# Optimization experiments

Measured on AMD Instinct MI355X. Metric: run time of the kernel, lower is better.

## Reference

```python
import jax, jax.numpy as jnp
import numpy as np

LAMBDA_D = 250.0
POS_MARGIN = 1.0
NEG_MARGIN = 0.2
BLOCK = 8          # block_size in the original
DIST_THRESH = 7.5  # correspondence threshold in pixels
EPS = 1e-12        # F.normalize eps


def _l2_normalize(x, axis):
    # matches torch.nn.functional.normalize: x / max(||x||_2, eps)
    n = jnp.linalg.norm(x, axis=axis, keepdims=True)
    return x / jnp.maximum(n, EPS)


def setup_inputs() -> dict:
    key = jax.random.key(0)
    k1, k2, k3 = jax.random.split(key, 3)
    b, d, hc, wc = 2, 256, 60, 80  # 480x640 image, block 8
    desc = jax.random.normal(k1, (b, d, hc, wc), dtype=jnp.float32)
    wrap_desc = jax.random.normal(k2, (b, d, hc, wc), dtype=jnp.float32)
    # realistic near-identity homographies (random H would warp everything off-image)
    H = jnp.eye(3, dtype=jnp.float32)[None] + 0.02 * jax.random.normal(k3, (b, 3, 3), dtype=jnp.float32)
    return {"desc": desc, "wrap_desc": wrap_desc, "H": H}


def reference(desc, wrap_desc, H):
    b, d, hc, wc = desc.shape
    n = hc * wc

    # cell-center coordinates in (row, col) order, shape (hc, wc, 2)
    coords = jnp.stack(
        jnp.meshgrid(jnp.arange(hc), jnp.arange(wc), indexing="ij"), axis=-1
    ).astype(jnp.float32) * BLOCK + BLOCK // 2

    # homogeneous (x, y, 1) points, shape (n, 3)
    xy1 = jnp.concatenate(
        [coords[..., 1:2], coords[..., 0:1], jnp.ones((hc, wc, 1), jnp.float32)],
        axis=-1,
    ).reshape(n, 3)

    # warp by homography: (b, n, 3)
    w = jnp.einsum("bij,nj->bni", H, xy1)
    wxy = w[..., :2] / w[..., 2:3]                       # (b, n, 2) in (x, y)
    warp = jnp.stack([wxy[..., 1], wxy[..., 0]], axis=-1).reshape(b, hc, wc, 2)  # (row, col)

    # distance between warped query centers and all cell centers: (b, hc, wc, hc, wc)
    dist = jnp.linalg.norm(coords[None, None, None] - warp[:, :, :, None, None, :], axis=-1)
    S = (dist <= DIST_THRESH).astype(desc.dtype)

    # unit-normalized descriptors, channel-last
    dn = _l2_normalize(jnp.transpose(desc, (0, 2, 3, 1)), axis=-1)       # (b, hc, wc, d)
    wn = _l2_normalize(jnp.transpose(wrap_desc, (0, 2, 3, 1)), axis=-1)  # (b, hc, wc, d)

    # full correlation volume via batched GEMM (same math as broadcast-sum)
    dot = jax.nn.relu(jnp.einsum("bijd,bkld->bijkl", dn, wn))           # (b,hc,wc,hc,wc)

    # normalize over warped-cell axis (k, l), then over query-cell axis (i, j)
    dot = _l2_normalize(dot.reshape(b, hc, wc, n), axis=3).reshape(b, hc, wc, hc, wc)
    dot = _l2_normalize(dot.reshape(b, n, hc, wc), axis=1).reshape(b, hc, wc, hc, wc)

    loss = LAMBDA_D * S * jax.nn.relu(POS_MARGIN - dot) + (1.0 - S) * jax.nn.relu(dot - NEG_MARGIN)
    # sum over (i,j,k,l) per image / n^2, then sum over batch == total sum / n^2
    return jnp.sum(loss) / float(n * n)
```

## Files before the change

kernel.cpp:

```cpp
#include <hip/hip_runtime.h>

#define HC 60
#define WCC 80
#define NCELL 4800
#define NP 4864
#define NB 38
#define DCH 256
#define BATCH 2
#define QT 64

typedef _Float16 half8 __attribute__((ext_vector_type(8)));
typedef float f32x4 __attribute__((ext_vector_type(4)));

__device__ __forceinline__ void gload_lds16(const void* gp, void* lp) {
  __builtin_amdgcn_global_load_lds(
      (const __attribute__((address_space(1))) void*)gp,
      (__attribute__((address_space(3))) void*)lp, 16, 0, 0);
}

__global__ __launch_bounds__(256) void warp_kernel(const float* __restrict__ H,
                                                   float* __restrict__ wout) {
  int idx = blockIdx.x * 256 + threadIdx.x;
  if (idx >= BATCH * NP) return;
  int b = idx / NP;
  int q = idx - b * NP;
  float wr = 1e9f, wc = 1e9f;
  if (q < NCELL) {
    int i = q / WCC;
    int j = q - i * WCC;
    float x = (float)(j * 8 + 4);
    float y = (float)(i * 8 + 4);
    const float* h = H + b * 9;
    float w0 = h[0] * x + h[1] * y + h[2];
    float w1 = h[3] * x + h[4] * y + h[5];
    float w2 = h[6] * x + h[7] * y + h[8];
    wr = w1 / w2;
    wc = w0 / w2;
  }
  wout[2 * idx]     = wr;
  wout[2 * idx + 1] = wc;
}

__global__ __launch_bounds__(256) void normalize_kernel(
    const float* __restrict__ desc, const float* __restrict__ wdesc,
    _Float16* __restrict__ dnp, _Float16* __restrict__ wnp) {
  __shared__ _Float16 vt[DCH][QT + 2];
  __shared__ float pss[4][QT];
  __shared__ float invq[QT];
  const int q0 = blockIdx.x * QT;
  const int which = blockIdx.y;
  const int b = blockIdx.z;
  const float* in = which ? wdesc : desc;
  _Float16* out = which ? wnp : dnp;
  const int tx = threadIdx.x & 63;
  const int ty = threadIdx.x >> 6;
  const int q = q0 + tx;
  float ss = 0.f;
  for (int cc = 0; cc < DCH / 4; ++cc) {
    const int c = cc * 4 + ty;
    float v = (q < NCELL) ? in[((size_t)b * DCH + c) * NCELL + q] : 0.f;
    vt[c][tx] = (_Float16)v;
    ss += v * v;
  }
  pss[ty][tx] = ss;
  __syncthreads();
  if (ty == 0) {
    float tot = pss[0][tx] + pss[1][tx] + pss[2][tx] + pss[3][tx];
    invq[tx] = 1.f / fmaxf(sqrtf(tot), 1e-12f);
  }
  __syncthreads();
  for (int it = 0; it < QT; ++it) {
    out[((size_t)b * NP + q0 + it) * DCH + threadIdx.x] =
        (_Float16)((float)vt[threadIdx.x][it] * invq[it]);
  }
}

template <int MODE>
__global__ __launch_bounds__(256) void gemm_kernel(
    const _Float16* __restrict__ A, const _Float16* __restrict__ Bm,
    const float* __restrict__ invr, const float* __restrict__ colscale,
    const float* __restrict__ warp, float* __restrict__ sqacc,
    float* __restrict__ lossp) {
  __shared__ _Float16 As[128][64];
  __shared__ _Float16 Bs[128][64];
  const int tid = threadIdx.x;
  const int wave = tid >> 6;
  const int lane = tid & 63;
  const int batch = blockIdx.z;
  const int row0 = blockIdx.y * 128;
  const int col0 = blockIdx.x * 128;
  const _Float16* Ab = A + ((size_t)batch * NP + row0) * DCH;
  const _Float16* Bb = Bm + ((size_t)batch * NP + col0) * DCH;

  const int wq_r = wave >> 1;
  const int wq_c = wave & 1;
  const int g = lane >> 4;
  const int cL = lane & 15;

  f32x4 acc[4][4] = {};

  const int srow = lane >> 3;
  const int scol = lane & 7;
  const int sc_swz = (scol ^ srow) * 8;

  for (int ks = 0; ks < 4; ++ks) {
#pragma unroll
    for (int c = 0; c < 4; ++c) {
      const int chunk = wave * 4 + c;
      const int r = chunk * 8 + srow;
      gload_lds16(Ab + (size_t)r * DCH + ks * 64 + sc_swz,
                  (char*)(&As[0][0]) + chunk * 1024);
      gload_lds16(Bb + (size_t)r * DCH + ks * 64 + sc_swz,
                  (char*)(&Bs[0][0]) + chunk * 1024);
    }
    __syncthreads();
#pragma unroll
    for (int kk = 0; kk < 2; ++kk) {
      half8 af[4], bf[4];
#pragma unroll
      for (int m = 0; m < 4; ++m) {
        const int row = wq_r * 64 + m * 16 + cL;
        const int c16 = (kk * 4 + g) ^ (row & 7);
        af[m] = *reinterpret_cast<const half8*>(
            (const char*)(&As[0][0]) + row * 128 + c16 * 16);
      }
#pragma unroll
      for (int n = 0; n < 4; ++n) {
        const int row = wq_c * 64 + n * 16 + cL;
        const int c16 = (kk * 4 + g) ^ (row & 7);
        bf[n] = *reinterpret_cast<const half8*>(
            (const char*)(&Bs[0][0]) + row * 128 + c16 * 16);
      }
#pragma unroll
      for (int m = 0; m < 4; ++m)
#pragma unroll
        for (int n = 0; n < 4; ++n)
          acc[m][n] =
              __builtin_amdgcn_mfma_f32_16x16x32_f16(af[m], bf[n], acc[m][n], 0, 0, 0);
    }
    __syncthreads();
  }

  if (MODE == 0 || MODE == 1) {
    float cs[4];
    if (MODE == 1) {
#pragma unroll
      for (int n = 0; n < 4; ++n)
        cs[n] = colscale[(size_t)batch * NP + col0 + wq_c * 64 + n * 16 + cL];
    }
    float rs[4][4];
#pragma unroll
    for (int m = 0; m < 4; ++m)
#pragma unroll
      for (int j = 0; j < 4; ++j) rs[m][j] = 0.f;
#pragma unroll
    for (int m = 0; m < 4; ++m)
#pragma unroll
      for (int n = 0; n < 4; ++n)
#pragma unroll
        for (int j = 0; j < 4; ++j) {
          float u = fmaxf(acc[m][n][j], 0.f);
          if (MODE == 1) u *= cs[n];
          rs[m][j] += u * u;
        }
#pragma unroll
    for (int m = 0; m < 4; ++m)
#pragma unroll
      for (int j = 0; j < 4; ++j) {
        float v = rs[m][j];
        v += __shfl_xor(v, 1, 64);
        v += __shfl_xor(v, 2, 64);
        v += __shfl_xor(v, 4, 64);
        v += __shfl_xor(v, 8, 64);
        if (cL == 0)
          atomicAdd(&sqacc[(size_t)batch * NP + row0 + wq_r * 64 + m * 16 + g * 4 + j], v);
      }
  } else {
    float cy[4], cx[4], ic[4];
    int cvalid[4];
#pragma unroll
    for (int n = 0; n < 4; ++n) {
      int ct = col0 + wq_c * 64 + n * 16 + cL;
      cvalid[n] = (ct < NCELL);
      int tk = ct / WCC;
      int tl = ct - tk * WCC;
      cy[n] = (float)(tk * 8 + 4);
      cx[n] = (float)(tl * 8 + 4);
      ic[n] = colscale[(size_t)batch * NP + ct];
    }
    float lsum = 0.f;
#pragma unroll
    for (int m = 0; m < 4; ++m)
#pragma unroll
      for (int j = 0; j < 4; ++j) {
        const int rq = row0 + wq_r * 64 + m * 16 + g * 4 + j;
        if (rq < NCELL) {
          const float ir = invr[(size_t)batch * NP + rq];
          const float wr = warp[((size_t)batch * NP + rq) * 2];
          const float wcol = warp[((size_t)batch * NP + rq) * 2 + 1];
#pragma unroll
          for (int n = 0; n < 4; ++n) {
            if (cvalid[n]) {
              float u = fmaxf(acc[m][n][j], 0.f);
              float v = u * ir * ic[n];
              float dr = cy[n] - wr;
              float dc = cx[n] - wcol;
              float pos = 250.f * fmaxf(1.f - v, 0.f);
              float neg = fmaxf(v - 0.2f, 0.f);
              lsum += (dr * dr + dc * dc <= 56.25f) ? pos : neg;
            }
          }
        }
      }
#pragma unroll
    for (int s = 1; s < 64; s <<= 1) lsum += __shfl_xor(lsum, s, 64);
    if (lane == 0) {
      int slot = (((batch * NB + blockIdx.y) * NB + blockIdx.x) << 2) | wave;
      lossp[slot] = lsum;
    }
  }
}

__global__ void finalize_inv(const float* __restrict__ sq, float* __restrict__ inv,
                             int count) {
  int i = blockIdx.x * 256 + threadIdx.x;
  if (i < count) inv[i] = 1.f / fmaxf(sqrtf(sq[i]), 1e-12f);
}

__global__ __launch_bounds__(1024) void loss_reduce(const float* __restrict__ lossp,
                                                    float* __restrict__ out) {
  const int COUNT = BATCH * NB * NB * 4;
  double s = 0.0;
  for (int i = threadIdx.x; i < COUNT; i += 1024) s += (double)lossp[i];
#pragma unroll
  for (int k = 1; k < 64; k <<= 1) s += __shfl_xor(s, k, 64);
  __shared__ double sd[16];
  if ((threadIdx.x & 63) == 0) sd[threadIdx.x >> 6] = s;
  __syncthreads();
  if (threadIdx.x == 0) {
    double t = 0.0;
    for (int w = 0; w < 16; ++w) t += sd[w];
    out[0] = (float)(t / ((double)NCELL * (double)NCELL));
  }
}

extern "C" void kernel_launch(void* const* d_in, const int* in_sizes, int n_in,
                              void* d_out, int out_size, void* d_ws, size_t ws_size,
                              hipStream_t stream) {
  const float* desc  = (const float*)d_in[0];
  const float* wdesc = (const float*)d_in[1];
  const float* H     = (const float*)d_in[2];
  char* ws = (char*)d_ws;

  constexpr size_t SZ_HALF = (size_t)BATCH * NP * DCH * sizeof(_Float16);
  constexpr size_t SZ_WARP = (size_t)BATCH * NP * 2 * sizeof(float);
  constexpr size_t SZ_VEC  = (size_t)BATCH * NP * sizeof(float);
  constexpr size_t SZ_LOSS = (size_t)BATCH * NB * NB * 4 * sizeof(float);
  constexpr size_t OFF_DNP  = 0;
  constexpr size_t OFF_WNP  = OFF_DNP + SZ_HALF;
  constexpr size_t OFF_WARP = OFF_WNP + SZ_HALF;
  constexpr size_t OFF_R2   = OFF_WARP + SZ_WARP;
  constexpr size_t OFF_INVR = OFF_R2 + SZ_VEC;
  constexpr size_t OFF_C2   = OFF_INVR + SZ_VEC;
  constexpr size_t OFF_INVC = OFF_C2 + SZ_VEC;
  constexpr size_t OFF_LOSS = OFF_INVC + SZ_VEC;

  _Float16* dnp = (_Float16*)(ws + OFF_DNP);
  _Float16* wnp = (_Float16*)(ws + OFF_WNP);
  float* warp = (float*)(ws + OFF_WARP);
  float* r2   = (float*)(ws + OFF_R2);
  float* invr = (float*)(ws + OFF_INVR);
  float* c2   = (float*)(ws + OFF_C2);
  float* invc = (float*)(ws + OFF_INVC);
  float* lossp = (float*)(ws + OFF_LOSS);

  hipMemsetAsync(r2, 0, SZ_VEC, stream);
  hipMemsetAsync(c2, 0, SZ_VEC, stream);

  warp_kernel<<<dim3((BATCH * NP + 255) / 256), 256, 0, stream>>>(H, warp);
  normalize_kernel<<<dim3(NP / QT, 2, BATCH), 256, 0, stream>>>(desc, wdesc, dnp, wnp);

  dim3 gg(NB, NB, BATCH);
  gemm_kernel<0><<<gg, 256, 0, stream>>>(dnp, wnp, nullptr, nullptr, nullptr, r2, nullptr);
  finalize_inv<<<(BATCH * NP + 255) / 256, 256, 0, stream>>>(r2, invr, BATCH * NP);
  gemm_kernel<1><<<gg, 256, 0, stream>>>(wnp, dnp, nullptr, invr, nullptr, c2, nullptr);
  finalize_inv<<<(BATCH * NP + 255) / 256, 256, 0, stream>>>(c2, invc, BATCH * NP);
  gemm_kernel<2><<<gg, 256, 0, stream>>>(dnp, wnp, invr, invc, warp, nullptr, lossp);
  loss_reduce<<<1, 1024, 0, stream>>>(lossp, (float*)d_out);
}
```

Before: 250.5 us.

## Materialize relu correlation once in fp16 and replace two GEMMs with streaming passes

The first GEMM now also writes the relu'd correlation volume as fp16 to a large workspace buffer. Two streaming kernels then read it back: one accumulates the column norms and one computes the loss. This replaces the second and third full GEMM recomputations with memory-bound reads of a buffer of about 95 MB. The GEMM main loop also gains double-buffered LDS staging so global loads overlap MFMA work. The change risks becoming bandwidth-bound and adds fp16 rounding of the stored dot values before normalization; the old path is kept when the workspace is too small.

```diff
diff --git a/kernel.cpp b/kernel.cpp
--- a/kernel.cpp
+++ b/kernel.cpp
@@ -10,6 +10,7 @@
 #define QT 64
 
 typedef _Float16 half8 __attribute__((ext_vector_type(8)));
+typedef _Float16 half2v __attribute__((ext_vector_type(2)));
 typedef float f32x4 __attribute__((ext_vector_type(4)));
 
 __device__ __forceinline__ void gload_lds16(const void* gp, void* lp) {
@@ -75,14 +76,14 @@
   }
 }
 
-template <int MODE>
+template <int MODE, bool STOREU>
 __global__ __launch_bounds__(256) void gemm_kernel(
     const _Float16* __restrict__ A, const _Float16* __restrict__ Bm,
     const float* __restrict__ invr, const float* __restrict__ colscale,
     const float* __restrict__ warp, float* __restrict__ sqacc,
-    float* __restrict__ lossp) {
-  __shared__ _Float16 As[128][64];
-  __shared__ _Float16 Bs[128][64];
+    float* __restrict__ lossp, _Float16* __restrict__ uout) {
+  __shared__ _Float16 As[2][128][64];
+  __shared__ _Float16 Bs[2][128][64];
   const int tid = threadIdx.x;
   const int wave = tid >> 6;
   const int lane = tid & 63;
@@ -103,17 +104,25 @@
   const int scol = lane & 7;
   const int sc_swz = (scol ^ srow) * 8;
 
-  for (int ks = 0; ks < 4; ++ks) {
+  auto stage = [&](int ks, int buf) {
 #pragma unroll
     for (int c = 0; c < 4; ++c) {
       const int chunk = wave * 4 + c;
       const int r = chunk * 8 + srow;
       gload_lds16(Ab + (size_t)r * DCH + ks * 64 + sc_swz,
-                  (char*)(&As[0][0]) + chunk * 1024);
+                  (char*)(&As[buf][0][0]) + chunk * 1024);
       gload_lds16(Bb + (size_t)r * DCH + ks * 64 + sc_swz,
-                  (char*)(&Bs[0][0]) + chunk * 1024);
-    }
-    __syncthreads();
+                  (char*)(&Bs[buf][0][0]) + chunk * 1024);
+    }
+  };
+
+  stage(0, 0);
+  __syncthreads();
+
+#pragma unroll
+  for (int ks = 0; ks < 4; ++ks) {
+    if (ks < 3) stage(ks + 1, (ks + 1) & 1);
+    const int buf = ks & 1;
 #pragma unroll
     for (int kk = 0; kk < 2; ++kk) {
       half8 af[4], bf[4];
@@ -122,14 +131,14 @@
         const int row = wq_r * 64 + m * 16 + cL;
         const int c16 = (kk * 4 + g) ^ (row & 7);
         af[m] = *reinterpret_cast<const half8*>(
-            (const char*)(&As[0][0]) + row * 128 + c16 * 16);
+            (const char*)(&As[buf][0][0]) + row * 128 + c16 * 16);
       }
 #pragma unroll
       for (int n = 0; n < 4; ++n) {
         const int row = wq_c * 64 + n * 16 + cL;
         const int c16 = (kk * 4 + g) ^ (row & 7);
         bf[n] = *reinterpret_cast<const half8*>(
-            (const char*)(&Bs[0][0]) + row * 128 + c16 * 16);
+            (const char*)(&Bs[buf][0][0]) + row * 128 + c16 * 16);
       }
 #pragma unroll
       for (int m = 0; m < 4; ++m)
@@ -175,7 +184,20 @@
         if (cL == 0)
           atomicAdd(&sqacc[(size_t)batch * NP + row0 + wq_r * 64 + m * 16 + g * 4 + j], v);
       }
-  } else {
+    if (STOREU) {
+#pragma unroll
+      for (int m = 0; m < 4; ++m)
+#pragma unroll
+        for (int j = 0; j < 4; ++j) {
+          const size_t r = (size_t)batch * NP + row0 + wq_r * 64 + m * 16 + g * 4 + j;
+#pragma unroll
+          for (int n = 0; n < 4; ++n) {
+            const int c = col0 + wq_c * 64 + n * 16 + cL;
+            uout[r * NP + c] = (_Float16)fmaxf(acc[m][n][j], 0.f);
+          }
+        }
+    }
+  } else if (MODE == 2) {
     float cy[4], cx[4], ic[4];
     int cvalid[4];
 #pragma unroll
@@ -221,6 +243,81 @@
   }
 }
 
+__global__ __launch_bounds__(256) void passB_kernel(const _Float16* __restrict__ u,
+                                                    const float* __restrict__ r2,
+                                                    float* __restrict__ c2) {
+  const int b = blockIdx.z;
+  const int t0 = blockIdx.x * 512 + threadIdx.x * 2;
+  if (t0 >= NP) return;
+  const int q0 = blockIdx.y * (NP / 64);
+  const _Float16* up = u + ((size_t)b * NP + q0) * NP + t0;
+  const float* r2p = r2 + b * NP + q0;
+  float s0 = 0.f, s1 = 0.f;
+  for (int q = 0; q < NP / 64; ++q) {
+    float ir = 1.f / fmaxf(sqrtf(r2p[q]), 1e-12f);
+    half2v h = *reinterpret_cast<const half2v*>(up);
+    float v0 = (float)h[0] * ir;
+    float v1 = (float)h[1] * ir;
+    s0 += v0 * v0;
+    s1 += v1 * v1;
+    up += NP;
+  }
+  atomicAdd(&c2[b * NP + t0], s0);
+  atomicAdd(&c2[b * NP + t0 + 1], s1);
+}
+
+__global__ __launch_bounds__(256) void passC_kernel(const _Float16* __restrict__ u,
+                                                    const float* __restrict__ r2,
+                                                    const float* __restrict__ c2,
+                                                    const float* __restrict__ warp,
+                                                    float* __restrict__ lossp) {
+  const int b = blockIdx.z;
+  const int t0 = blockIdx.x * 512 + threadIdx.x * 2;
+  const int q0 = blockIdx.y * (NP / 32);
+  float cy[2], cx[2], ic[2];
+  bool val[2];
+#pragma unroll
+  for (int i = 0; i < 2; ++i) {
+    const int t = t0 + i;
+    const bool v = (t0 < NP) && (t < NCELL);
+    val[i] = v;
+    const int tk = t / WCC;
+    const int tl = t - tk * WCC;
+    cy[i] = (float)(tk * 8 + 4);
+    cx[i] = (float)(tl * 8 + 4);
+    ic[i] = v ? 1.f / fmaxf(sqrtf(c2[b * NP + t]), 1e-12f) : 0.f;
+  }
+  float lsum = 0.f;
+  if (t0 < NP) {
+    const _Float16* up = u + ((size_t)b * NP + q0) * NP + t0;
+    for (int q = 0; q < NP / 32; ++q) {
+      const int qq = q0 + q;
+      const float ir = 1.f / fmaxf(sqrtf(r2[b * NP + qq]), 1e-12f);
+      const float wr = warp[(size_t)(b * NP + qq) * 2];
+      const float wc = warp[(size_t)(b * NP + qq) * 2 + 1];
+      half2v h = *reinterpret_cast<const half2v*>(up);
+#pragma unroll
+      for (int i = 0; i < 2; ++i) {
+        if (val[i]) {
+          float v = (float)h[i] * ir * ic[i];
+          float dr = cy[i] - wr;
+          float dc = cx[i] - wc;
+          float pos = 250.f * fmaxf(1.f - v, 0.f);
+          float neg = fmaxf(v - 0.2f, 0.f);
+          lsum += (dr * dr + dc * dc <= 56.25f) ? pos : neg;
+        }
+      }
+      up += NP;
+    }
+  }
+#pragma unroll
+  for (int s = 1; s < 64; s <<= 1) lsum += __shfl_xor(lsum, s, 64);
+  if ((threadIdx.x & 63) == 0) {
+    int slot = ((((b * 32 + blockIdx.y) * 10 + blockIdx.x) << 2) | (threadIdx.x >> 6));
+    lossp[slot] = lsum;
+  }
+}
+
 __global__ void finalize_inv(const float* __restrict__ sq, float* __restrict__ inv,
                              int count) {
   int i = blockIdx.x * 256 + threadIdx.x;
@@ -228,10 +325,9 @@
 }
 
 __global__ __launch_bounds__(1024) void loss_reduce(const float* __restrict__ lossp,
-                                                    float* __restrict__ out) {
-  const int COUNT = BATCH * NB * NB * 4;
+                                                    float* __restrict__ out, int count) {
   double s = 0.0;
-  for (int i = threadIdx.x; i < COUNT; i += 1024) s += (double)lossp[i];
+  for (int i = threadIdx.x; i < count; i += 1024) s += (double)lossp[i];
 #pragma unroll
   for (int k = 1; k < 64; k <<= 1) s += __shfl_xor(s, k, 64);
   __shared__ double sd[16];
@@ -256,6 +352,7 @@
   constexpr size_t SZ_WARP = (size_t)BATCH * NP * 2 * sizeof(float);
   constexpr size_t SZ_VEC  = (size_t)BATCH * NP * sizeof(float);
   constexpr size_t SZ_LOSS = (size_t)BATCH * NB * NB * 4 * sizeof(float);
+  constexpr size_t SZ_U    = (size_t)BATCH * NP * NP * sizeof(_Float16);
   constexpr size_t OFF_DNP  = 0;
   constexpr size_t OFF_WNP  = OFF_DNP + SZ_HALF;
   constexpr size_t OFF_WARP = OFF_WNP + SZ_HALF;
@@ -264,6 +361,8 @@
   constexpr size_t OFF_C2   = OFF_INVR + SZ_VEC;
   constexpr size_t OFF_INVC = OFF_C2 + SZ_VEC;
   constexpr size_t OFF_LOSS = OFF_INVC + SZ_VEC;
+  constexpr size_t OFF_U    = OFF_LOSS + SZ_LOSS;
+  constexpr size_t TOTAL    = OFF_U + SZ_U;
 
   _Float16* dnp = (_Float16*)(ws + OFF_DNP);
   _Float16* wnp = (_Float16*)(ws + OFF_WNP);
@@ -273,18 +372,29 @@
   float* c2   = (float*)(ws + OFF_C2);
   float* invc = (float*)(ws + OFF_INVC);
   float* lossp = (float*)(ws + OFF_LOSS);
-
-  hipMemsetAsync(r2, 0, SZ_VEC, stream);
-  hipMemsetAsync(c2, 0, SZ_VEC, stream);
+  _Float16* u = (_Float16*)(ws + OFF_U);
+
+  hipMemsetAsync(r2, 0, 4 * SZ_VEC, stream);
 
   warp_kernel<<<dim3((BATCH * NP + 255) / 256), 256, 0, stream>>>(H, warp);
   normalize_kernel<<<dim3(NP / QT, 2, BATCH), 256, 0, stream>>>(desc, wdesc, dnp, wnp);
 
   dim3 gg(NB, NB, BATCH);
-  gemm_kernel<0><<<gg, 256, 0, stream>>>(dnp, wnp, nullptr, nullptr, nullptr, r2, nullptr);
-  finalize_inv<<<(BATCH * NP + 255) / 256, 256, 0, stream>>>(r2, invr, BATCH * NP);
-  gemm_kernel<1><<<gg, 256, 0, stream>>>(wnp, dnp, nullptr, invr, nullptr, c2, nullptr);
-  finalize_inv<<<(BATCH * NP + 255) / 256, 256, 0, stream>>>(c2, invc, BATCH * NP);
-  gemm_kernel<2><<<gg, 256, 0, stream>>>(dnp, wnp, invr, invc, warp, nullptr, lossp);
-  loss_reduce<<<1, 1024, 0, stream>>>(lossp, (float*)d_out);
-}
+  if (ws_size >= TOTAL) {
+    gemm_kernel<0, true><<<gg, 256, 0, stream>>>(dnp, wnp, nullptr, nullptr, nullptr,
+                                                 r2, nullptr, u);
+    passB_kernel<<<dim3(10, 64, BATCH), 256, 0, stream>>>(u, r2, c2);
+    passC_kernel<<<dim3(10, 32, BATCH), 256, 0, stream>>>(u, r2, c2, warp, lossp);
+    loss_reduce<<<1, 1024, 0, stream>>>(lossp, (float*)d_out, BATCH * 32 * 10 * 4);
+  } else {
+    gemm_kernel<0, false><<<gg, 256, 0, stream>>>(dnp, wnp, nullptr, nullptr, nullptr,
+                                                  r2, nullptr, nullptr);
+    finalize_inv<<<(BATCH * NP + 255) / 256, 256, 0, stream>>>(r2, invr, BATCH * NP);
+    gemm_kernel<1, false><<<gg, 256, 0, stream>>>(wnp, dnp, nullptr, invr, nullptr,
+                                                  c2, nullptr, nullptr);
+    finalize_inv<<<(BATCH * NP + 255) / 256, 256, 0, stream>>>(c2, invc, BATCH * NP);
+    gemm_kernel<2, false><<<gg, 256, 0, stream>>>(dnp, wnp, invr, invc, warp,
+                                                  nullptr, lossp, nullptr);
+    loss_reduce<<<1, 1024, 0, stream>>>(lossp, (float*)d_out, BATCH * NB * NB * 4);
+  }
+}
```

New measurement: 268.3 us. +7.1%, slower.

## Load GEMM fragments directly from global memory instead of staging through LDS

Applied to the files above, without the earlier changes.

The GEMM kernels stop staging A/B tiles in shared memory with global_load_lds and barriers. Each wave now reads its MFMA fragments straight from global memory as 16-byte vectors, with the K loop fully unrolled. This removes LDS traffic and __syncthreads, at the cost of redundant global/L2 reads across waves, since each row is loaded by two waves. The two memsets are merged into one covering r2, invr, c2 and invc.

```diff
diff --git a/kernel.cpp b/kernel.cpp
--- a/kernel.cpp
+++ b/kernel.cpp
@@ -11,12 +11,6 @@
 
 typedef _Float16 half8 __attribute__((ext_vector_type(8)));
 typedef float f32x4 __attribute__((ext_vector_type(4)));
-
-__device__ __forceinline__ void gload_lds16(const void* gp, void* lp) {
-  __builtin_amdgcn_global_load_lds(
-      (const __attribute__((address_space(1))) void*)gp,
-      (__attribute__((address_space(3))) void*)lp, 16, 0, 0);
-}
 
 __global__ __launch_bounds__(256) void warp_kernel(const float* __restrict__ H,
                                                    float* __restrict__ wout) {
@@ -81,64 +75,40 @@
     const float* __restrict__ invr, const float* __restrict__ colscale,
     const float* __restrict__ warp, float* __restrict__ sqacc,
     float* __restrict__ lossp) {
-  __shared__ _Float16 As[128][64];
-  __shared__ _Float16 Bs[128][64];
   const int tid = threadIdx.x;
   const int wave = tid >> 6;
   const int lane = tid & 63;
   const int batch = blockIdx.z;
   const int row0 = blockIdx.y * 128;
   const int col0 = blockIdx.x * 128;
-  const _Float16* Ab = A + ((size_t)batch * NP + row0) * DCH;
-  const _Float16* Bb = Bm + ((size_t)batch * NP + col0) * DCH;
 
   const int wq_r = wave >> 1;
   const int wq_c = wave & 1;
   const int g = lane >> 4;
   const int cL = lane & 15;
 
+  const _Float16* ap =
+      A + ((size_t)batch * NP + row0 + wq_r * 64 + cL) * DCH + g * 8;
+  const _Float16* bp =
+      Bm + ((size_t)batch * NP + col0 + wq_c * 64 + cL) * DCH + g * 8;
+
   f32x4 acc[4][4] = {};
 
-  const int srow = lane >> 3;
-  const int scol = lane & 7;
-  const int sc_swz = (scol ^ srow) * 8;
-
-  for (int ks = 0; ks < 4; ++ks) {
-#pragma unroll
-    for (int c = 0; c < 4; ++c) {
-      const int chunk = wave * 4 + c;
-      const int r = chunk * 8 + srow;
-      gload_lds16(Ab + (size_t)r * DCH + ks * 64 + sc_swz,
-                  (char*)(&As[0][0]) + chunk * 1024);
-      gload_lds16(Bb + (size_t)r * DCH + ks * 64 + sc_swz,
-                  (char*)(&Bs[0][0]) + chunk * 1024);
-    }
-    __syncthreads();
-#pragma unroll
-    for (int kk = 0; kk < 2; ++kk) {
-      half8 af[4], bf[4];
-#pragma unroll
-      for (int m = 0; m < 4; ++m) {
-        const int row = wq_r * 64 + m * 16 + cL;
-        const int c16 = (kk * 4 + g) ^ (row & 7);
-        af[m] = *reinterpret_cast<const half8*>(
-            (const char*)(&As[0][0]) + row * 128 + c16 * 16);
-      }
-#pragma unroll
-      for (int n = 0; n < 4; ++n) {
-        const int row = wq_c * 64 + n * 16 + cL;
-        const int c16 = (kk * 4 + g) ^ (row & 7);
-        bf[n] = *reinterpret_cast<const half8*>(
-            (const char*)(&Bs[0][0]) + row * 128 + c16 * 16);
-      }
-#pragma unroll
-      for (int m = 0; m < 4; ++m)
-#pragma unroll
-        for (int n = 0; n < 4; ++n)
-          acc[m][n] =
-              __builtin_amdgcn_mfma_f32_16x16x32_f16(af[m], bf[n], acc[m][n], 0, 0, 0);
-    }
-    __syncthreads();
+#pragma unroll
+  for (int ks = 0; ks < 8; ++ks) {
+    half8 af[4], bf[4];
+#pragma unroll
+    for (int m = 0; m < 4; ++m)
+      af[m] = *reinterpret_cast<const half8*>(ap + (size_t)m * 16 * DCH + ks * 32);
+#pragma unroll
+    for (int n = 0; n < 4; ++n)
+      bf[n] = *reinterpret_cast<const half8*>(bp + (size_t)n * 16 * DCH + ks * 32);
+#pragma unroll
+    for (int m = 0; m < 4; ++m)
+#pragma unroll
+      for (int n = 0; n < 4; ++n)
+        acc[m][n] =
+            __builtin_amdgcn_mfma_f32_16x16x32_f16(af[m], bf[n], acc[m][n], 0, 0, 0);
   }
 
   if (MODE == 0 || MODE == 1) {
@@ -228,10 +198,9 @@
 }
 
 __global__ __launch_bounds__(1024) void loss_reduce(const float* __restrict__ lossp,
-                                                    float* __restrict__ out) {
-  const int COUNT = BATCH * NB * NB * 4;
+                                                    float* __restrict__ out, int count) {
   double s = 0.0;
-  for (int i = threadIdx.x; i < COUNT; i += 1024) s += (double)lossp[i];
+  for (int i = threadIdx.x; i < count; i += 1024) s += (double)lossp[i];
 #pragma unroll
   for (int k = 1; k < 64; k <<= 1) s += __shfl_xor(s, k, 64);
   __shared__ double sd[16];
@@ -255,7 +224,6 @@
   constexpr size_t SZ_HALF = (size_t)BATCH * NP * DCH * sizeof(_Float16);
   constexpr size_t SZ_WARP = (size_t)BATCH * NP * 2 * sizeof(float);
   constexpr size_t SZ_VEC  = (size_t)BATCH * NP * sizeof(float);
-  constexpr size_t SZ_LOSS = (size_t)BATCH * NB * NB * 4 * sizeof(float);
   constexpr size_t OFF_DNP  = 0;
   constexpr size_t OFF_WNP  = OFF_DNP + SZ_HALF;
   constexpr size_t OFF_WARP = OFF_WNP + SZ_HALF;
@@ -274,8 +242,7 @@
   float* invc = (float*)(ws + OFF_INVC);
   float* lossp = (float*)(ws + OFF_LOSS);
 
-  hipMemsetAsync(r2, 0, SZ_VEC, stream);
-  hipMemsetAsync(c2, 0, SZ_VEC, stream);
+  hipMemsetAsync(r2, 0, 4 * SZ_VEC, stream);
 
   warp_kernel<<<dim3((BATCH * NP + 255) / 256), 256, 0, stream>>>(H, warp);
   normalize_kernel<<<dim3(NP / QT, 2, BATCH), 256, 0, stream>>>(desc, wdesc, dnp, wnp);
@@ -286,5 +253,5 @@
   gemm_kernel<1><<<gg, 256, 0, stream>>>(wnp, dnp, nullptr, invr, nullptr, c2, nullptr);
   finalize_inv<<<(BATCH * NP + 255) / 256, 256, 0, stream>>>(c2, invc, BATCH * NP);
   gemm_kernel<2><<<gg, 256, 0, stream>>>(dnp, wnp, invr, invc, warp, nullptr, lossp);
-  loss_reduce<<<1, 1024, 0, stream>>>(lossp, (float*)d_out);
-}
+  loss_reduce<<<1, 1024, 0, stream>>>(lossp, (float*)d_out, BATCH * NB * NB * 4);
+}
```

Result: slower. 405.1 us (+61.7%).

## Use 256x256 double-buffered GEMM tiles and fold inverse-norm finalize into consumers

Applied to the files above, without the earlier changes.

Doubles the GEMM block tile to 256x256 with 512 threads (8 waves, each computing 128x64), raising operand reuse per LDS load and cutting the number of blocks. It also double-buffers the async global-to-LDS staging so the next K slice loads while the current one is multiplied. The separate finalize_inv kernels are removed: consumers now compute 1/max(sqrt(sum),eps) inline from the raw squared sums, and the two memsets are merged into one. In exchange it uses 64KB of LDS per block and many more accumulator registers, which lowers occupancy. The grid also shrinks to 722 blocks, which risks tail imbalance across the CUs.

```diff
diff --git a/kernel.cpp b/kernel.cpp
--- a/kernel.cpp
+++ b/kernel.cpp
@@ -4,7 +4,7 @@
 #define WCC 80
 #define NCELL 4800
 #define NP 4864
-#define NB 38
+#define NTB 19
 #define DCH 256
 #define BATCH 2
 #define QT 64
@@ -76,63 +76,69 @@
 }
 
 template <int MODE>
-__global__ __launch_bounds__(256) void gemm_kernel(
+__global__ __launch_bounds__(512, 2) void gemm_kernel(
     const _Float16* __restrict__ A, const _Float16* __restrict__ Bm,
-    const float* __restrict__ invr, const float* __restrict__ colscale,
+    const float* __restrict__ rowsq, const float* __restrict__ colsq,
     const float* __restrict__ warp, float* __restrict__ sqacc,
     float* __restrict__ lossp) {
-  __shared__ _Float16 As[128][64];
-  __shared__ _Float16 Bs[128][64];
+  __shared__ _Float16 As[2][256][64];
+  __shared__ _Float16 Bs[2][256][64];
   const int tid = threadIdx.x;
   const int wave = tid >> 6;
   const int lane = tid & 63;
   const int batch = blockIdx.z;
-  const int row0 = blockIdx.y * 128;
-  const int col0 = blockIdx.x * 128;
+  const int row0 = blockIdx.y * 256;
+  const int col0 = blockIdx.x * 256;
   const _Float16* Ab = A + ((size_t)batch * NP + row0) * DCH;
   const _Float16* Bb = Bm + ((size_t)batch * NP + col0) * DCH;
 
-  const int wq_r = wave >> 1;
-  const int wq_c = wave & 1;
+  const int wr = wave >> 2;
+  const int wc = wave & 3;
   const int g = lane >> 4;
   const int cL = lane & 15;
 
-  f32x4 acc[4][4] = {};
+  f32x4 acc[8][4] = {};
 
   const int srow = lane >> 3;
   const int scol = lane & 7;
   const int sc_swz = (scol ^ srow) * 8;
 
-  for (int ks = 0; ks < 4; ++ks) {
+  auto stage = [&](int ks, int buf) {
 #pragma unroll
     for (int c = 0; c < 4; ++c) {
       const int chunk = wave * 4 + c;
       const int r = chunk * 8 + srow;
       gload_lds16(Ab + (size_t)r * DCH + ks * 64 + sc_swz,
-                  (char*)(&As[0][0]) + chunk * 1024);
+                  (char*)(&As[buf][0][0]) + chunk * 1024);
       gload_lds16(Bb + (size_t)r * DCH + ks * 64 + sc_swz,
-                  (char*)(&Bs[0][0]) + chunk * 1024);
-    }
-    __syncthreads();
+                  (char*)(&Bs[buf][0][0]) + chunk * 1024);
+    }
+  };
+
+  stage(0, 0);
+  __syncthreads();
+  for (int ks = 0; ks < 4; ++ks) {
+    if (ks < 3) stage(ks + 1, (ks + 1) & 1);
+    const int buf = ks & 1;
 #pragma unroll
     for (int kk = 0; kk < 2; ++kk) {
-      half8 af[4], bf[4];
-#pragma unroll
-      for (int m = 0; m < 4; ++m) {
-        const int row = wq_r * 64 + m * 16 + cL;
+      half8 af[8], bf[4];
+#pragma unroll
+      for (int m = 0; m < 8; ++m) {
+        const int row = wr * 128 + m * 16 + cL;
         const int c16 = (kk * 4 + g) ^ (row & 7);
         af[m] = *reinterpret_cast<const half8*>(
-            (const char*)(&As[0][0]) + row * 128 + c16 * 16);
+            (const char*)(&As[buf][0][0]) + row * 128 + c16 * 16);
       }
 #pragma unroll
       for (int n = 0; n < 4; ++n) {
-        const int row = wq_c * 64 + n * 16 + cL;
+        const int row = wc * 64 + n * 16 + cL;
         const int c16 = (kk * 4 + g) ^ (row & 7);
         bf[n] = *reinterpret_cast<const half8*>(
-            (const char*)(&Bs[0][0]) + row * 128 + c16 * 16);
-      }
-#pragma unroll
-      for (int m = 0; m < 4; ++m)
+            (const char*)(&Bs[buf][0][0]) + row * 128 + c16 * 16);
+      }
+#pragma unroll
+      for (int m = 0; m < 8; ++m)
 #pragma unroll
         for (int n = 0; n < 4; ++n)
           acc[m][n] =
@@ -145,16 +151,18 @@
     float cs[4];
     if (MODE == 1) {
 #pragma unroll
-      for (int n = 0; n < 4; ++n)
-        cs[n] = colscale[(size_t)batch * NP + col0 + wq_c * 64 + n * 16 + cL];
-    }
-    float rs[4][4];
-#pragma unroll
-    for (int m = 0; m < 4; ++m)
+      for (int n = 0; n < 4; ++n) {
+        float v = colsq[(size_t)batch * NP + col0 + wc * 64 + n * 16 + cL];
+        cs[n] = 1.f / fmaxf(sqrtf(v), 1e-12f);
+      }
+    }
+    float rs[8][4];
+#pragma unroll
+    for (int m = 0; m < 8; ++m)
 #pragma unroll
       for (int j = 0; j < 4; ++j) rs[m][j] = 0.f;
 #pragma unroll
-    for (int m = 0; m < 4; ++m)
+    for (int m = 0; m < 8; ++m)
 #pragma unroll
       for (int n = 0; n < 4; ++n)
 #pragma unroll
@@ -164,7 +172,7 @@
           rs[m][j] += u * u;
         }
 #pragma unroll
-    for (int m = 0; m < 4; ++m)
+    for (int m = 0; m < 8; ++m)
 #pragma unroll
       for (int j = 0; j < 4; ++j) {
         float v = rs[m][j];
@@ -173,37 +181,38 @@
         v += __shfl_xor(v, 4, 64);
         v += __shfl_xor(v, 8, 64);
         if (cL == 0)
-          atomicAdd(&sqacc[(size_t)batch * NP + row0 + wq_r * 64 + m * 16 + g * 4 + j], v);
+          atomicAdd(&sqacc[(size_t)batch * NP + row0 + wr * 128 + m * 16 + g * 4 + j], v);
       }
   } else {
     float cy[4], cx[4], ic[4];
     int cvalid[4];
 #pragma unroll
     for (int n = 0; n < 4; ++n) {
-      int ct = col0 + wq_c * 64 + n * 16 + cL;
+      int ct = col0 + wc * 64 + n * 16 + cL;
       cvalid[n] = (ct < NCELL);
       int tk = ct / WCC;
       int tl = ct - tk * WCC;
       cy[n] = (float)(tk * 8 + 4);
       cx[n] = (float)(tl * 8 + 4);
-      ic[n] = colscale[(size_t)batch * NP + ct];
+      ic[n] = 1.f / fmaxf(sqrtf(colsq[(size_t)batch * NP + ct]), 1e-12f);
     }
     float lsum = 0.f;
 #pragma unroll
-    for (int m = 0; m < 4; ++m)
+    for (int m = 0; m < 8; ++m)
 #pragma unroll
       for (int j = 0; j < 4; ++j) {
-        const int rq = row0 + wq_r * 64 + m * 16 + g * 4 + j;
+        const int rq = row0 + wr * 128 + m * 16 + g * 4 + j;
         if (rq < NCELL) {
-          const float ir = invr[(size_t)batch * NP + rq];
-          const float wr = warp[((size_t)batch * NP + rq) * 2];
+          const float ir =
+              1.f / fmaxf(sqrtf(rowsq[(size_t)batch * NP + rq]), 1e-12f);
+          const float wrr = warp[((size_t)batch * NP + rq) * 2];
           const float wcol = warp[((size_t)batch * NP + rq) * 2 + 1];
 #pragma unroll
           for (int n = 0; n < 4; ++n) {
             if (cvalid[n]) {
               float u = fmaxf(acc[m][n][j], 0.f);
               float v = u * ir * ic[n];
-              float dr = cy[n] - wr;
+              float dr = cy[n] - wrr;
               float dc = cx[n] - wcol;
               float pos = 250.f * fmaxf(1.f - v, 0.f);
               float neg = fmaxf(v - 0.2f, 0.f);
@@ -215,23 +224,16 @@
 #pragma unroll
     for (int s = 1; s < 64; s <<= 1) lsum += __shfl_xor(lsum, s, 64);
     if (lane == 0) {
-      int slot = (((batch * NB + blockIdx.y) * NB + blockIdx.x) << 2) | wave;
+      int slot = (((batch * NTB + blockIdx.y) * NTB + blockIdx.x) << 3) | wave;
       lossp[slot] = lsum;
     }
   }
 }
 
-__global__ void finalize_inv(const float* __restrict__ sq, float* __restrict__ inv,
-                             int count) {
-  int i = blockIdx.x * 256 + threadIdx.x;
-  if (i < count) inv[i] = 1.f / fmaxf(sqrtf(sq[i]), 1e-12f);
-}
-
 __global__ __launch_bounds__(1024) void loss_reduce(const float* __restrict__ lossp,
-                                                    float* __restrict__ out) {
-  const int COUNT = BATCH * NB * NB * 4;
+                                                    float* __restrict__ out, int count) {
   double s = 0.0;
-  for (int i = threadIdx.x; i < COUNT; i += 1024) s += (double)lossp[i];
+  for (int i = threadIdx.x; i < count; i += 1024) s += (double)lossp[i];
 #pragma unroll
   for (int k = 1; k < 64; k <<= 1) s += __shfl_xor(s, k, 64);
   __shared__ double sd[16];
@@ -255,36 +257,28 @@
   constexpr size_t SZ_HALF = (size_t)BATCH * NP * DCH * sizeof(_Float16);
   constexpr size_t SZ_WARP = (size_t)BATCH * NP * 2 * sizeof(float);
   constexpr size_t SZ_VEC  = (size_t)BATCH * NP * sizeof(float);
-  constexpr size_t SZ_LOSS = (size_t)BATCH * NB * NB * 4 * sizeof(float);
   constexpr size_t OFF_DNP  = 0;
   constexpr size_t OFF_WNP  = OFF_DNP + SZ_HALF;
   constexpr size_t OFF_WARP = OFF_WNP + SZ_HALF;
   constexpr size_t OFF_R2   = OFF_WARP + SZ_WARP;
-  constexpr size_t OFF_INVR = OFF_R2 + SZ_VEC;
-  constexpr size_t OFF_C2   = OFF_INVR + SZ_VEC;
-  constexpr size_t OFF_INVC = OFF_C2 + SZ_VEC;
-  constexpr size_t OFF_LOSS = OFF_INVC + SZ_VEC;
+  constexpr size_t OFF_C2   = OFF_R2 + SZ_VEC;
+  constexpr size_t OFF_LOSS = OFF_C2 + SZ_VEC;
 
   _Float16* dnp = (_Float16*)(ws + OFF_DNP);
   _Float16* wnp = (_Float16*)(ws + OFF_WNP);
   float* warp = (float*)(ws + OFF_WARP);
   float* r2   = (float*)(ws + OFF_R2);
-  float* invr = (float*)(ws + OFF_INVR);
   float* c2   = (float*)(ws + OFF_C2);
-  float* invc = (float*)(ws + OFF_INVC);
   float* lossp = (float*)(ws + OFF_LOSS);
 
-  hipMemsetAsync(r2, 0, SZ_VEC, stream);
-  hipMemsetAsync(c2, 0, SZ_VEC, stream);
+  hipMemsetAsync(r2, 0, 2 * SZ_VEC, stream);
 
   warp_kernel<<<dim3((BATCH * NP + 255) / 256), 256, 0, stream>>>(H, warp);
   normalize_kernel<<<dim3(NP / QT, 2, BATCH), 256, 0, stream>>>(desc, wdesc, dnp, wnp);
 
-  dim3 gg(NB, NB, BATCH);
-  gemm_kernel<0><<<gg, 256, 0, stream>>>(dnp, wnp, nullptr, nullptr, nullptr, r2, nullptr);
-  finalize_inv<<<(BATCH * NP + 255) / 256, 256, 0, stream>>>(r2, invr, BATCH * NP);
-  gemm_kernel<1><<<gg, 256, 0, stream>>>(wnp, dnp, nullptr, invr, nullptr, c2, nullptr);
-  finalize_inv<<<(BATCH * NP + 255) / 256, 256, 0, stream>>>(c2, invc, BATCH * NP);
-  gemm_kernel<2><<<gg, 256, 0, stream>>>(dnp, wnp, invr, invc, warp, nullptr, lossp);
-  loss_reduce<<<1, 1024, 0, stream>>>(lossp, (float*)d_out);
-}
+  dim3 gg(NTB, NTB, BATCH);
+  gemm_kernel<0><<<gg, 512, 0, stream>>>(dnp, wnp, nullptr, nullptr, nullptr, r2, nullptr);
+  gemm_kernel<1><<<gg, 512, 0, stream>>>(wnp, dnp, nullptr, r2, nullptr, c2, nullptr);
+  gemm_kernel<2><<<gg, 512, 0, stream>>>(dnp, wnp, r2, c2, warp, nullptr, lossp);
+  loss_reduce<<<1, 1024, 0, stream>>>(lossp, (float*)d_out, BATCH * NTB * NTB * 8);
+}
```

Result: slower. 284.2 us (+13.4%).
